# Kernel optimization log

Measured on AMD Instinct MI355X. Metric: run time of the kernel, lower is better.

## Reference

```python
import jax, jax.numpy as jnp
import numpy as np

USER_NUM, ITEM_NUM, D, E, B = 50000, 20000, 64, 2_000_000, 16384
N = USER_NUM + ITEM_NUM


def setup_inputs() -> dict:
    key = jax.random.key(0)
    ks = jax.random.split(key, 20)
    return {
        "user_emb": jax.random.normal(ks[0], (USER_NUM, D), jnp.float32),
        "item_emb": jax.random.normal(ks[1], (ITEM_NUM, D), jnp.float32),
        "edge_row": jax.random.randint(ks[2], (E,), 0, N, jnp.int32),
        "edge_col": jax.random.randint(ks[3], (E,), 0, N, jnp.int32),
        "edge_val": jax.random.uniform(ks[4], (E,), jnp.float32),
        "Wg1": jax.random.normal(ks[5], (D, D), jnp.float32) * 0.05,
        "bg1": jax.random.normal(ks[6], (D,), jnp.float32) * 0.05,
        "Wg2": jax.random.normal(ks[7], (D, D), jnp.float32) * 0.05,
        "bg2": jax.random.normal(ks[8], (D,), jnp.float32) * 0.05,
        "W1": jax.random.normal(ks[9], (4 * D, D), jnp.float32) * 0.05,
        "b1": jax.random.normal(ks[10], (D,), jnp.float32) * 0.05,
        "W2": jax.random.normal(ks[11], (D, 32), jnp.float32) * 0.05,
        "b2": jax.random.normal(ks[12], (32,), jnp.float32) * 0.05,
        "W3": jax.random.normal(ks[13], (32, 1), jnp.float32) * 0.05,
        "b3": jax.random.normal(ks[14], (1,), jnp.float32) * 0.05,
        "userID": jax.random.randint(ks[15], (B,), 0, USER_NUM, jnp.int32),
        "itemID": jax.random.randint(ks[16], (B,), 0, ITEM_NUM, jnp.int32),
    }


def _spmm(row, col, val, x):
    # sparse [N,N] @ dense [N,D] via gather + segment_sum
    msgs = val[:, None] * x[col]  # [E, D]
    return jax.ops.segment_sum(msgs, row, num_segments=N)


def reference(user_emb, item_emb, edge_row, edge_col, edge_val,
              Wg1, bg1, Wg2, bg2, W1, b1, W2, b2, W3, b3, userID, itemID):
    features = jnp.concatenate([user_emb, item_emb], axis=0)  # [N, D]
    final = features
    # single GCN layer (layers=[64,64]); L1 = L + I so SpMM(L1,x) = SpMM(L,x) + x
    lx = _spmm(edge_row, edge_col, edge_val, features)
    lx2 = _spmm(edge_row, edge_col, edge_val, features * features)
    inter1 = (lx + features) @ Wg1 + bg1
    inter2 = lx2 @ Wg2 + bg2
    h = jax.nn.leaky_relu(inter1 + inter2, negative_slope=0.01)
    final = jnp.concatenate([final, h], axis=1)  # [N, 2D]

    u = final[userID]                     # [B, 2D]
    i = final[itemID + USER_NUM]          # [B, 2D]
    embed = jnp.concatenate([u, i], axis=1)  # [B, 4D]
    embed = jax.nn.relu(embed @ W1 + b1)
    embed = jax.nn.relu(embed @ W2 + b2)
    embed = embed @ W3 + b3
    return embed.reshape(-1)
```

## Files before the change

### kernel.cpp

```cpp
#include <hip/hip_runtime.h>
#include <hip/hip_bf16.h>

#define USER_NUM 50000
#define ITEM_NUM 20000
#define NNODE    70000
#define DD       64
#define CHUNK    1024
#define NCHUNK   ((NNODE + CHUNK - 1) / CHUNK)
#define APB      1024
#define NS2      128
#define T_CAP    32768
#define NCHUNK2  (T_CAP / CHUNK)
#define GCAP     327680

__device__ __forceinline__ const float* feat_row(const float* __restrict__ ue,
                                                 const float* __restrict__ ie, int n) {
    return (n < USER_NUM) ? (ue + (size_t)n * DD)
                          : (ie + (size_t)(n - USER_NUM) * DD);
}


__global__ __launch_bounds__(256) void zero_kernel(int* __restrict__ cnt2,
                                                   int* __restrict__ tmask,
                                                   int* __restrict__ gcur) {
    const int tid    = blockIdx.x * 256 + (int)threadIdx.x;
    const int stride = gridDim.x * 256;
    for (int i = tid; i < T_CAP; i += stride) cnt2[i] = 0;
    for (int i = tid; i < NNODE; i += stride) tmask[i] = 0;
    if (tid < 8) gcur[tid] = tid * GCAP;
}


__global__ __launch_bounds__(256) void mark_kernel(const int* __restrict__ uid,
                                                   const int* __restrict__ iid,
                                                   int* __restrict__ tmask, int B) {
    const int stride = gridDim.x * blockDim.x;
    for (int s = blockIdx.x * blockDim.x + threadIdx.x; s < B; s += stride) {
        tmask[uid[s]] = 1;
        tmask[USER_NUM + iid[s]] = 1;
    }
}


__global__ __launch_bounds__(256) void chunksum_kernel(const int* __restrict__ arr,
                                                       int* __restrict__ csum, int N) {
    __shared__ int red[4];
    const int c = blockIdx.x;
    const int t = threadIdx.x;
    int s = 0;
#pragma unroll
    for (int i = 0; i < 4; ++i) {
        const int idx = c * CHUNK + t + 256 * i;
        s += (idx < N) ? arr[idx] : 0;
    }
#pragma unroll
    for (int off = 32; off; off >>= 1) s += __shfl_down(s, off);
    if ((t & 63) == 0) red[t >> 6] = s;
    __syncthreads();
    if (t == 0) csum[c] = red[0] + red[1] + red[2] + red[3];
}

__global__ __launch_bounds__(128) void scan_small_kernel(const int* __restrict__ csum,
                                                         int* __restrict__ coff,
                                                         int NC) {
    __shared__ int s[128];
    const int t = threadIdx.x;
    const int v = (t < NC) ? csum[t] : 0;
    s[t] = v;
    __syncthreads();
    for (int off = 1; off < 128; off <<= 1) {
        const int val = s[t];
        const int add = (t >= off) ? s[t - off] : 0;
        __syncthreads();
        s[t] = val + add;
        __syncthreads();
    }
    if (t < NC) coff[t] = s[t] - v;
}

__global__ __launch_bounds__(256) void fill_flags_kernel(
    const int* __restrict__ tmask, const int* __restrict__ coff,
    int* __restrict__ cmapx, int* __restrict__ nodes, int* __restrict__ meta) {
    __shared__ int sp[256];
    const int c  = blockIdx.x;
    const int t  = threadIdx.x;
    const int g0 = c * CHUNK + t * 4;
    int v[4];
#pragma unroll
    for (int i = 0; i < 4; ++i) v[i] = (g0 + i < NNODE) ? tmask[g0 + i] : 0;
    const int s = ((v[0] + v[1]) + (v[2] + v[3]));
    sp[t] = s;
    __syncthreads();
    for (int off = 1; off < 256; off <<= 1) {
        const int val = sp[t];
        const int add = (t >= off) ? sp[t - off] : 0;
        __syncthreads();
        sp[t] = val + add;
        __syncthreads();
    }
    int run = coff[c] + sp[t] - s;
#pragma unroll
    for (int i = 0; i < 4; ++i) {
        const int g = g0 + i;
        if (g < NNODE) {
            cmapx[g] = v[i] ? run : -1;
            if (v[i]) nodes[run] = g;
            if (g == USER_NUM) meta[1] = run;
            run += v[i];
        } else if (g == NNODE) {
            meta[0] = run;
        }
    }
    if (g0 + 4 == NNODE) meta[0] = run;
}

__global__ __launch_bounds__(256) void fill_kernel(const int* __restrict__ cnt,
                                                   const int* __restrict__ coff,
                                                   int* __restrict__ base,
                                                   int* __restrict__ cursor, int N) {
    __shared__ int sp[256];
    const int c  = blockIdx.x;
    const int t  = threadIdx.x;
    const int g0 = c * CHUNK + t * 4;
    int v[4];
#pragma unroll
    for (int i = 0; i < 4; ++i) v[i] = (g0 + i < N) ? cnt[g0 + i] : 0;
    const int s = ((v[0] + v[1]) + (v[2] + v[3]));
    sp[t] = s;
    __syncthreads();
    for (int off = 1; off < 256; off <<= 1) {
        const int val = sp[t];
        const int add = (t >= off) ? sp[t - off] : 0;
        __syncthreads();
        sp[t] = val + add;
        __syncthreads();
    }
    int run = coff[c] + sp[t] - s;
#pragma unroll
    for (int i = 0; i < 4; ++i) {
        const int g = g0 + i;
        if (g < N) {
            base[g]   = run;
            cursor[g] = run;
            run += v[i];
        }
    }
    if (g0 + 4 == N) base[N] = run;
}


__global__ __launch_bounds__(256) void append_kernel(
    const int* __restrict__ erow, const int* __restrict__ ecol,
    const float* __restrict__ eval, const int* __restrict__ cmapx,
    int* __restrict__ gcur, int* __restrict__ grow, int2* __restrict__ gpair,
    int* __restrict__ cnt2, int E) {
    __shared__ int lcnt[8];
    __shared__ int lbase[8];
    const int t = threadIdx.x;
    if (t < 8) lcnt[t] = 0;
    __syncthreads();
    const int e0 = blockIdx.x * APB + t;
    int sl[4], c[4], gr[4], rk[4];
    float v[4];
#pragma unroll
    for (int i = 0; i < 4; ++i) {
        const int e = e0 + 256 * i;
        gr[i] = -1;
        if (e < E) {
            const int r = erow[e];
            const int slot = cmapx[r];
            if (slot >= 0) {
                sl[i] = slot;
                c[i]  = ecol[e];
                v[i]  = eval[e];
                gr[i] = (r * 8) / NNODE;
                rk[i] = atomicAdd(&lcnt[gr[i]], 1);
            }
        }
    }
    __syncthreads();
    if (t < 8 && lcnt[t] > 0) lbase[t] = atomicAdd(&gcur[t], lcnt[t]);
    __syncthreads();
#pragma unroll
    for (int i = 0; i < 4; ++i) {
        if (gr[i] >= 0) {
            const int pos = lbase[gr[i]] + rk[i];
            grow[pos]  = sl[i];
            gpair[pos] = make_int2(c[i], __float_as_int(v[i]));
            atomicAdd(&cnt2[sl[i]], 1);
        }
    }
}


__global__ __launch_bounds__(256) void scatter2_kernel(
    const int* __restrict__ grow, const int2* __restrict__ gpair,
    const int* __restrict__ gcur, int* __restrict__ cursor2,
    int2* __restrict__ epair) {
    const int g    = blockIdx.x & 7;
    const int rank = blockIdx.x >> 3;
    const int hi = gcur[g];
    for (int i = g * GCAP + rank * 256 + (int)threadIdx.x; i < hi; i += NS2 * 256) {
        const int slot = grow[i];
        const int pos = atomicAdd(&cursor2[slot], 1);
        epair[pos] = gpair[i];
    }
}


__global__ __launch_bounds__(256) void spmm_kernel(
    const float* __restrict__ ue, const float* __restrict__ ie,
    const int2* __restrict__ epair, const int* __restrict__ base2,
    const int* __restrict__ nodes, const int* __restrict__ meta,
    float* __restrict__ lx, float* __restrict__ lx2) {
    const int T = meta[0];
    const int lane = threadIdx.x & 63;
    int wv = (int)((blockIdx.x * blockDim.x + threadIdx.x) >> 6);
    wv = __builtin_amdgcn_readfirstlane(wv);
    const int nw = (int)((gridDim.x * blockDim.x) >> 6);
    for (int r = wv; r < T; r += nw) {
        const int jb = base2[r];
        const int je = base2[r + 1];
        float acc1 = 0.f, acc2 = 0.f;
        int j = jb;
        for (; j + 8 <= je; j += 8) {
            int2 p[8];
#pragma unroll
            for (int t = 0; t < 8; ++t) p[t] = epair[j + t];
            float f[8];
#pragma unroll
            for (int t = 0; t < 8; ++t) f[t] = feat_row(ue, ie, p[t].x)[lane];
#pragma unroll
            for (int t = 0; t < 8; ++t) {
                const float v = __int_as_float(p[t].y);
                acc1 = fmaf(v, f[t], acc1);
                acc2 = fmaf(v * f[t], f[t], acc2);
            }
        }
        for (; j + 4 <= je; j += 4) {
            int2 p[4];
#pragma unroll
            for (int t = 0; t < 4; ++t) p[t] = epair[j + t];
            float f[4];
#pragma unroll
            for (int t = 0; t < 4; ++t) f[t] = feat_row(ue, ie, p[t].x)[lane];
#pragma unroll
            for (int t = 0; t < 4; ++t) {
                const float v = __int_as_float(p[t].y);
                acc1 = fmaf(v, f[t], acc1);
                acc2 = fmaf(v * f[t], f[t], acc2);
            }
        }
        for (; j < je; ++j) {
            const int2 p = epair[j];
            const float f = feat_row(ue, ie, p.x)[lane];
            const float v = __int_as_float(p.y);
            acc1 = fmaf(v, f, acc1);
            acc2 = fmaf(v * f, f, acc2);
        }
        const int n = nodes[r];
        lx [(size_t)r * DD + lane] = acc1 + feat_row(ue, ie, n)[lane];
        lx2[(size_t)r * DD + lane] = acc2;
    }
}


template <int IS_USER>
__global__ __launch_bounds__(256) void xform_fused_kernel(
    const float* __restrict__ lx, const float* __restrict__ lx2,
    const float* __restrict__ fb,
    const float* __restrict__ Wg1, const float* __restrict__ Wg2,
    const float* __restrict__ bg1, const float* __restrict__ bg2,
    const float* __restrict__ W1, const float* __restrict__ b1,
    float* __restrict__ part,
    const int* __restrict__ nodes, const int* __restrict__ meta) {
    const int Tu = meta[1];
    const int T  = meta[0];
    const int start = IS_USER ? 0  : Tu;
    const int lim   = IS_USER ? Tu : T;
    const int tb = start + (int)blockIdx.x * 64;
    if (tb >= lim) return;

    __shared__ float sXa[64 * DD];
    __shared__ float sXb[64 * DD];
    __shared__ float sP [64 * DD];
    const int t     = threadIdx.x;
    const int lane  = t & 63;
    const int w     = t >> 6;
    const int khalf = (w & 1) * 32;
    const int rhalf = (w >> 1) * 32;

    float wva[32], wvb[32];
#pragma unroll
    for (int k = 0; k < 32; ++k) {
        wva[k] = Wg1[(khalf + k) * DD + lane];
        wvb[k] = Wg2[(khalf + k) * DD + lane];
    }

    float4* sXav = (float4*)sXa;
    float4* sXbv = (float4*)sXb;
    float4* sPv  = (float4*)sP;
#pragma unroll
    for (int i = 0; i < 4; ++i) {
        const int f4  = t + 256 * i;
        const int row = f4 >> 4;
        const int c   = f4 & 15;
        const int g   = min(tb + row, lim - 1);
        sXav[f4] = ((const float4*)(lx  + (size_t)g * DD))[c];
        sXbv[f4] = ((const float4*)(lx2 + (size_t)g * DD))[c];
        sPv[f4]  = make_float4(0.f, 0.f, 0.f, 0.f);
    }
    __syncthreads();

#pragma unroll 2
    for (int r = 0; r < 32; ++r) {
        const int row = rhalf + r;
        const float* ra = &sXa[row * DD + khalf];
        const float* rb = &sXb[row * DD + khalf];
        float o0 = 0.f, o1 = 0.f, o2 = 0.f, o3 = 0.f;
#pragma unroll
        for (int q = 0; q < 8; ++q) {
            const float4 qa = *(const float4*)(ra + 4 * q);
            const float4 qb = *(const float4*)(rb + 4 * q);
            o0 = fmaf(qa.x, wva[4 * q + 0], o0);
            o1 = fmaf(qa.y, wva[4 * q + 1], o1);
            o0 = fmaf(qa.z, wva[4 * q + 2], o0);
            o1 = fmaf(qa.w, wva[4 * q + 3], o1);
            o2 = fmaf(qb.x, wvb[4 * q + 0], o2);
            o3 = fmaf(qb.y, wvb[4 * q + 1], o3);
            o2 = fmaf(qb.z, wvb[4 * q + 2], o2);
            o3 = fmaf(qb.w, wvb[4 * q + 3], o3);
        }
        atomicAdd(&sP[row * DD + lane], (o0 + o1) + (o2 + o3));
    }
    __syncthreads();

#pragma unroll
    for (int i = 0; i < 4; ++i) {
        const int f4  = t + 256 * i;
        const int row = f4 >> 4;
        const int c   = f4 & 15;
        float4 v = sPv[f4];
        const float4 ba = ((const float4*)bg1)[c];
        const float4 bb = ((const float4*)bg2)[c];
        v.x += ba.x + bb.x; v.y += ba.y + bb.y;
        v.z += ba.z + bb.z; v.w += ba.w + bb.w;
        v.x = (v.x > 0.f) ? v.x : 0.01f * v.x;
        v.y = (v.y > 0.f) ? v.y : 0.01f * v.y;
        v.z = (v.z > 0.f) ? v.z : 0.01f * v.z;
        v.w = (v.w > 0.f) ? v.w : 0.01f * v.w;
        sXav[f4] = v;
        sPv[f4]  = make_float4(0.f, 0.f, 0.f, 0.f);
        const int g = min(tb + row, lim - 1);
        int n = nodes[g];
        if (!IS_USER) n -= USER_NUM;
        sXbv[f4] = ((const float4*)(fb + (size_t)n * DD))[c];
    }

    const float* W1a = W1 + (IS_USER ? 0 : 2 * DD * DD);
    const float* W1b = W1a + DD * DD;
#pragma unroll
    for (int k = 0; k < 32; ++k) {
        wva[k] = W1b[(khalf + k) * DD + lane];
        wvb[k] = W1a[(khalf + k) * DD + lane];
    }
    __syncthreads();

#pragma unroll 2
    for (int r = 0; r < 32; ++r) {
        const int row = rhalf + r;
        const float* ra = &sXa[row * DD + khalf];
        const float* rb = &sXb[row * DD + khalf];
        float o0 = 0.f, o1 = 0.f, o2 = 0.f, o3 = 0.f;
#pragma unroll
        for (int q = 0; q < 8; ++q) {
            const float4 qa = *(const float4*)(ra + 4 * q);
            const float4 qb = *(const float4*)(rb + 4 * q);
            o0 = fmaf(qa.x, wva[4 * q + 0], o0);
            o1 = fmaf(qa.y, wva[4 * q + 1], o1);
            o0 = fmaf(qa.z, wva[4 * q + 2], o0);
            o1 = fmaf(qa.w, wva[4 * q + 3], o1);
            o2 = fmaf(qb.x, wvb[4 * q + 0], o2);
            o3 = fmaf(qb.y, wvb[4 * q + 1], o3);
            o2 = fmaf(qb.z, wvb[4 * q + 2], o2);
            o3 = fmaf(qb.w, wvb[4 * q + 3], o3);
        }
        atomicAdd(&sP[row * DD + lane], (o0 + o1) + (o2 + o3));
    }
    __syncthreads();

    float4* outv = (float4*)part;
#pragma unroll
    for (int i = 0; i < 4; ++i) {
        const int f4  = t + 256 * i;
        const int row = f4 >> 4;
        const int c   = f4 & 15;
        const int g   = tb + row;
        float4 v = sPv[f4];
        if (IS_USER) {
            const float4 b = ((const float4*)b1)[c];
            v.x += b.x; v.y += b.y; v.z += b.z; v.w += b.w;
        }
        if (g < lim) outv[(size_t)g * 16 + c] = v;
    }
}


__global__ __launch_bounds__(256) void mlp_kernel(
    const float* __restrict__ part, const int* __restrict__ cmapx,
    const float* __restrict__ W2, const float* __restrict__ b2,
    const float* __restrict__ W3, const float* __restrict__ b3,
    const int* __restrict__ uid, const int* __restrict__ iid,
    float* __restrict__ out, int B) {
    __shared__ float sW2[DD * 32];
    __shared__ float sW3[32];
    for (int i = threadIdx.x; i < DD * 32; i += 256) sW2[i] = W2[i];
    if (threadIdx.x < 32) sW3[threadIdx.x] = W3[threadIdx.x];
    __syncthreads();
    const int lane = threadIdx.x & 63;
    const int wave = (int)((blockIdx.x * blockDim.x + threadIdx.x) >> 6);
    const int nw   = (int)((gridDim.x * blockDim.x) >> 6);
    const float bias2 = b2[lane & 31];
    const float w3v   = sW3[lane & 31];
    const float bias3 = b3[0];
    for (int s = wave; s < B; s += nw) {
        const int su = cmapx[uid[s]];
        const int si = cmapx[USER_NUM + iid[s]];
        const float pu = part[(size_t)su * DD + lane];
        const float pi = part[(size_t)si * DD + lane];
        const float x  = pu + pi;
        const float o1 = (x > 0.f) ? x : 0.f;
        float acc_a = bias2, acc_b = 0.f;
#pragma unroll
        for (int k = 0; k < DD; k += 2) {
            acc_a = fmaf(__shfl(o1, k),     sW2[k * 32 + (lane & 31)],       acc_a);
            acc_b = fmaf(__shfl(o1, k + 1), sW2[(k + 1) * 32 + (lane & 31)], acc_b);
        }
        const float a2 = acc_a + acc_b;
        const float o2 = (a2 > 0.f) ? a2 : 0.f;
        float p = o2 * w3v;
        p += __shfl_xor(p, 1);
        p += __shfl_xor(p, 2);
        p += __shfl_xor(p, 4);
        p += __shfl_xor(p, 8);
        p += __shfl_xor(p, 16);
        if (lane == 0) out[s] = p + bias3;
    }
}

extern "C" void kernel_launch(void* const* d_in, const int* in_sizes, int n_in,
                              void* d_out, int out_size, void* d_ws, size_t ws_size,
                              hipStream_t stream) {
    const float* ue   = (const float*)d_in[0];
    const float* ie   = (const float*)d_in[1];
    const int*   erow = (const int*)d_in[2];
    const int*   ecol = (const int*)d_in[3];
    const float* evalp= (const float*)d_in[4];
    const float* Wg1  = (const float*)d_in[5];
    const float* bg1  = (const float*)d_in[6];
    const float* Wg2  = (const float*)d_in[7];
    const float* bg2  = (const float*)d_in[8];
    const float* W1   = (const float*)d_in[9];
    const float* b1   = (const float*)d_in[10];
    const float* W2   = (const float*)d_in[11];
    const float* b2   = (const float*)d_in[12];
    const float* W3   = (const float*)d_in[13];
    const float* b3   = (const float*)d_in[14];
    const int*   uid  = (const int*)d_in[15];
    const int*   iid  = (const int*)d_in[16];
    float* out = (float*)d_out;

    const int E = in_sizes[2];
    const int B = in_sizes[15];

    const int TU_MAX = (B < USER_NUM) ? B : USER_NUM;
    const int TI_MAX = (B < ITEM_NUM) ? B : ITEM_NUM;

    char* ws = (char*)d_ws;
    const size_t ndc = (size_t)T_CAP * DD;
    float* lx    = (float*)ws;
    float* lx2   = lx + ndc;
    float* part  = lx2 + ndc;
    int*   grow  = (int*)ws;
    int2*  gpair = (int2*)(ws + 11u * 1024 * 1024);
    char*  tail  = ws + 32u * 1024 * 1024;
    int2*  epair = (int2*)tail;
    int*   mi    = (int*)(tail + (size_t)E * sizeof(int2));
    int*   cnt2    = mi;
    int*   cursor2 = cnt2 + T_CAP;
    int*   base2   = cursor2 + T_CAP;
    int*   tmask   = base2 + T_CAP + 1;
    int*   cmapx   = tmask + NNODE;
    int*   nodes   = cmapx + NNODE;
    int*   csum    = nodes + T_CAP;
    int*   coff    = csum + 128;
    int*   gcur    = coff + 128;
    int*   meta    = gcur + 8;

    zero_kernel<<<512, 256, 0, stream>>>(cnt2, tmask, gcur);
    mark_kernel<<<(B + 255) / 256, 256, 0, stream>>>(uid, iid, tmask, B);
    chunksum_kernel<<<NCHUNK, 256, 0, stream>>>(tmask, csum, NNODE);
    scan_small_kernel<<<1, 128, 0, stream>>>(csum, coff, NCHUNK);
    fill_flags_kernel<<<NCHUNK, 256, 0, stream>>>(tmask, coff, cmapx, nodes, meta);
    append_kernel<<<(E + APB - 1) / APB, 256, 0, stream>>>(
        erow, ecol, evalp, cmapx, gcur, grow, gpair, cnt2, E);
    chunksum_kernel<<<NCHUNK2, 256, 0, stream>>>(cnt2, csum, T_CAP);
    scan_small_kernel<<<1, 128, 0, stream>>>(csum, coff, NCHUNK2);
    fill_kernel<<<NCHUNK2, 256, 0, stream>>>(cnt2, coff, base2, cursor2, T_CAP);
    scatter2_kernel<<<8 * NS2, 256, 0, stream>>>(grow, gpair, gcur, cursor2, epair);
    spmm_kernel<<<4096, 256, 0, stream>>>(ue, ie, epair, base2, nodes, meta,
                                          lx, lx2);

    xform_fused_kernel<1><<<(TU_MAX + 63) / 64, 256, 0, stream>>>(
        lx, lx2, ue, Wg1, Wg2, bg1, bg2, W1, b1, part, nodes, meta);
    xform_fused_kernel<0><<<(TI_MAX + 63) / 64, 256, 0, stream>>>(
        lx, lx2, ie, Wg1, Wg2, bg1, bg2, W1, b1, part, nodes, meta);

    mlp_kernel<<<1024, 256, 0, stream>>>(part, cmapx, W2, b2, W3, b3,
                                         uid, iid, out, B);
}
```

Before: 246.7 us.

## Move per-slot edge histogram out of append into LDS-privatized pass

Removes the per-edge global atomicAdd on cnt2 from the append kernel. A new hist3 kernel instead counts slot occurrences per row group in shared memory and flushes them to global. Group slot boundaries come from gslot, which fill_flags now records. The append kernel also processes 8 edges per thread instead of 4 with half as many blocks. The cost is an extra kernel launch and a second read of grow. Shared memory is sized GROWS (8750 ints), which assumes a group's slot span never exceeds the number of nodes in that group.

```diff
diff --git a/kernel.cpp b/kernel.cpp
--- a/kernel.cpp
+++ b/kernel.cpp
@@ -7,8 +7,11 @@
 #define DD       64
 #define CHUNK    1024
 #define NCHUNK   ((NNODE + CHUNK - 1) / CHUNK)
-#define APB      1024
+#define GROWS    (NNODE / 8)
+#define APB      2048
+#define EPT      8
 #define NS2      128
+#define NB3      16
 #define T_CAP    32768
 #define NCHUNK2  (T_CAP / CHUNK)
 #define GCAP     327680
@@ -80,7 +83,8 @@
 
 __global__ __launch_bounds__(256) void fill_flags_kernel(
     const int* __restrict__ tmask, const int* __restrict__ coff,
-    int* __restrict__ cmapx, int* __restrict__ nodes, int* __restrict__ meta) {
+    int* __restrict__ cmapx, int* __restrict__ nodes, int* __restrict__ meta,
+    int* __restrict__ gslot) {
     __shared__ int sp[256];
     const int c  = blockIdx.x;
     const int t  = threadIdx.x;
@@ -106,12 +110,14 @@
             cmapx[g] = v[i] ? run : -1;
             if (v[i]) nodes[run] = g;
             if (g == USER_NUM) meta[1] = run;
+            if (g % GROWS == 0) gslot[g / GROWS] = run;
             run += v[i];
         } else if (g == NNODE) {
             meta[0] = run;
-        }
-    }
-    if (g0 + 4 == NNODE) meta[0] = run;
+            gslot[8] = run;
+        }
+    }
+    if (g0 + 4 == NNODE) { meta[0] = run; gslot[8] = run; }
 }
 
 __global__ __launch_bounds__(256) void fill_kernel(const int* __restrict__ cnt,
@@ -153,17 +159,17 @@
     const int* __restrict__ erow, const int* __restrict__ ecol,
     const float* __restrict__ eval, const int* __restrict__ cmapx,
     int* __restrict__ gcur, int* __restrict__ grow, int2* __restrict__ gpair,
-    int* __restrict__ cnt2, int E) {
+    int E) {
     __shared__ int lcnt[8];
     __shared__ int lbase[8];
     const int t = threadIdx.x;
     if (t < 8) lcnt[t] = 0;
     __syncthreads();
     const int e0 = blockIdx.x * APB + t;
-    int sl[4], c[4], gr[4], rk[4];
-    float v[4];
-#pragma unroll
-    for (int i = 0; i < 4; ++i) {
+    int sl[EPT], c[EPT], gr[EPT], rk[EPT];
+    float v[EPT];
+#pragma unroll
+    for (int i = 0; i < EPT; ++i) {
         const int e = e0 + 256 * i;
         gr[i] = -1;
         if (e < E) {
@@ -182,13 +188,34 @@
     if (t < 8 && lcnt[t] > 0) lbase[t] = atomicAdd(&gcur[t], lcnt[t]);
     __syncthreads();
 #pragma unroll
-    for (int i = 0; i < 4; ++i) {
+    for (int i = 0; i < EPT; ++i) {
         if (gr[i] >= 0) {
             const int pos = lbase[gr[i]] + rk[i];
             grow[pos]  = sl[i];
             gpair[pos] = make_int2(c[i], __float_as_int(v[i]));
-            atomicAdd(&cnt2[sl[i]], 1);
-        }
+        }
+    }
+}
+
+
+__global__ __launch_bounds__(256) void hist3_kernel(const int* __restrict__ grow,
+                                                    const int* __restrict__ gcur,
+                                                    const int* __restrict__ gslot,
+                                                    int* __restrict__ cnt2) {
+    __shared__ int hloc[GROWS];
+    const int g    = blockIdx.x & 7;
+    const int rank = blockIdx.x >> 3;
+    const int slo  = gslot[g];
+    const int span = gslot[g + 1] - slo;
+    for (int i = threadIdx.x; i < span; i += 256) hloc[i] = 0;
+    __syncthreads();
+    const int hi = gcur[g];
+    for (int i = g * GCAP + rank * 256 + (int)threadIdx.x; i < hi; i += NB3 * 256)
+        atomicAdd(&hloc[grow[i] - slo], 1);
+    __syncthreads();
+    for (int i = threadIdx.x; i < span; i += 256) {
+        const int v = hloc[i];
+        if (v) atomicAdd(&cnt2[slo + i], v);
     }
 }
 
@@ -496,14 +523,17 @@
     int*   coff    = csum + 128;
     int*   gcur    = coff + 128;
     int*   meta    = gcur + 8;
+    int*   gslot   = meta + 8;
 
     zero_kernel<<<512, 256, 0, stream>>>(cnt2, tmask, gcur);
     mark_kernel<<<(B + 255) / 256, 256, 0, stream>>>(uid, iid, tmask, B);
     chunksum_kernel<<<NCHUNK, 256, 0, stream>>>(tmask, csum, NNODE);
     scan_small_kernel<<<1, 128, 0, stream>>>(csum, coff, NCHUNK);
-    fill_flags_kernel<<<NCHUNK, 256, 0, stream>>>(tmask, coff, cmapx, nodes, meta);
+    fill_flags_kernel<<<NCHUNK, 256, 0, stream>>>(tmask, coff, cmapx, nodes,
+                                                  meta, gslot);
     append_kernel<<<(E + APB - 1) / APB, 256, 0, stream>>>(
-        erow, ecol, evalp, cmapx, gcur, grow, gpair, cnt2, E);
+        erow, ecol, evalp, cmapx, gcur, grow, gpair, E);
+    hist3_kernel<<<8 * NB3, 256, 0, stream>>>(grow, gcur, gslot, cnt2);
     chunksum_kernel<<<NCHUNK2, 256, 0, stream>>>(cnt2, csum, T_CAP);
     scan_small_kernel<<<1, 128, 0, stream>>>(csum, coff, NCHUNK2);
     fill_kernel<<<NCHUNK2, 256, 0, stream>>>(cnt2, coff, base2, cursor2, T_CAP);
```

Result: faster. 230.7 us (-6.5%).
